# Kernel optimization log

Measured on AMD Instinct MI355X. Metric: run time of the kernel, lower is better.

## Reference

```python
import jax, jax.numpy as jnp
import numpy as np

NUM_HEADS = 16
HEAD_DIM = 64
LORA_SCALE = 1.0 / 8.0  # lora_alpha (1) / r (8), loralib defaults


def setup_inputs() -> dict:
    key = jax.random.key(0)
    ks = jax.random.split(key, 10)
    B, N, C = 4, 2048, 1024
    O = 3 * NUM_HEADS * HEAD_DIM  # 3072
    s = lambda fan: 1.0 / np.sqrt(fan)
    return {
        "x": jax.random.normal(ks[0], (B, N, C), jnp.float32),
        "W_qkv": jax.random.normal(ks[1], (O, C), jnp.float32) * s(C),
        "W_lora": jax.random.normal(ks[2], (O, C), jnp.float32) * s(C),
        "b_lora": jax.random.normal(ks[3], (O,), jnp.float32) * s(C),
        "A_q": jax.random.normal(ks[4], (8, C), jnp.float32) * s(C),
        "B_q": jnp.zeros((NUM_HEADS * HEAD_DIM, 8), jnp.float32) + jax.random.normal(ks[5], (NUM_HEADS * HEAD_DIM, 8), jnp.float32) * 0.02,
        "A_v": jax.random.normal(ks[6], (8, C), jnp.float32) * s(C),
        "B_v": jax.random.normal(ks[7], (NUM_HEADS * HEAD_DIM, 8), jnp.float32) * 0.02,
        "W_out": jax.random.normal(ks[8], (C, NUM_HEADS * HEAD_DIM), jnp.float32) * s(NUM_HEADS * HEAD_DIM),
        "b_out": jax.random.normal(ks[9], (C,), jnp.float32) * s(NUM_HEADS * HEAD_DIM),
    }


def reference(x, W_qkv, W_lora, b_lora, A_q, B_q, A_v, B_v, W_out, b_out):
    B, N, C = x.shape
    H, D = NUM_HEADS, HEAD_DIM
    scale = D ** (-0.5)

    def split_qkv(t):
        t = t.reshape(B, N, 3, H, D).transpose(2, 0, 3, 1, 4)
        return t[0], t[1], t[2]

    q, k, v = split_qkv(jnp.einsum('bnc,oc->bno', x, W_qkv))
    ql, _, vl = split_qkv(jnp.einsum('bnc,oc->bno', x, W_lora) + b_lora)

    # low-rank LoRA updates for Q and V slices only (K disabled)
    dq = (jnp.einsum('bnc,rc->bnr', x, A_q) @ B_q.T) * LORA_SCALE  # (B,N,HD)
    dv = (jnp.einsum('bnc,rc->bnr', x, A_v) @ B_v.T) * LORA_SCALE
    dq = dq.reshape(B, N, H, D).transpose(0, 2, 1, 3)
    dv = dv.reshape(B, N, H, D).transpose(0, 2, 1, 3)

    q = q + ql + dq
    v = v + vl + dv

    attn = jax.nn.softmax(jnp.einsum('bhnd,bhmd->bhnm', q, k) * scale, axis=-1)
    out = jnp.einsum('bhnm,bhmd->bhnd', attn, v)
    out = out.transpose(0, 2, 1, 3).reshape(B, N, H * D)  # b h n d -> b n (h d)
    return jnp.einsum('bnk,ck->bnc', out, W_out) + b_out
```

## Files before the change

kernel.cpp:

```cpp
#include <hip/hip_runtime.h>
#include <hip/hip_bf16.h>

typedef unsigned short u16;
typedef unsigned int u32;
typedef __attribute__((ext_vector_type(8))) short bf16x8;
typedef __attribute__((ext_vector_type(4))) float f32x4;

#define GLDS16(gptr, lptr)                                                        \
  __builtin_amdgcn_global_load_lds(                                               \
      (__attribute__((address_space(1))) const void*)(gptr),                      \
      (__attribute__((address_space(3))) void*)(lptr), 16, 0, 0)

__device__ __forceinline__ u16 f2bf(float f) {
  union { float f; unsigned u; } v; v.f = f;
  unsigned r = v.u + 0x7fffu + ((v.u >> 16) & 1u);
  return (u16)(r >> 16);
}

__device__ __forceinline__ u32 pack_bf2(float a, float b) {
  union { __hip_bfloat162 h2; u32 u; } v;
  v.h2 = __float22bfloat162_rn(make_float2(a, b));
  return v.u;
}

__global__ void k_f32_to_bf16(const float* __restrict__ in, u16* __restrict__ out, int n4) {
  int i = blockIdx.x * 256 + threadIdx.x;
  if (i < n4) {
    float4 f = reinterpret_cast<const float4*>(in)[i];
    ushort4 u;
    u.x = f2bf(f.x); u.y = f2bf(f.y); u.z = f2bf(f.z); u.w = f2bf(f.w);
    reinterpret_cast<ushort4*>(out)[i] = u;
  }
}

__global__ void k_prep_weff(const float* __restrict__ Wqkv, const float* __restrict__ Wlora,
                            const float* __restrict__ blora,
                            const float* __restrict__ Aq, const float* __restrict__ Bq,
                            const float* __restrict__ Av, const float* __restrict__ Bv,
                            u16* __restrict__ Weff, float* __restrict__ beff) {
  int idx = blockIdx.x * 256 + threadIdx.x;
  int o = idx >> 10, c = idx & 1023;
  float w = Wqkv[idx];
  if (o < 1024) {
    float lr = 0.f;
#pragma unroll
    for (int r = 0; r < 8; ++r) lr += Bq[o * 8 + r] * Aq[r * 1024 + c];
    w += Wlora[idx] + 0.125f * lr;
  } else if (o >= 2048) {
    int o2 = o - 2048;
    float lr = 0.f;
#pragma unroll
    for (int r = 0; r < 8; ++r) lr += Bv[o2 * 8 + r] * Av[r * 1024 + c];
    w += Wlora[idx] + 0.125f * lr;
  }
  Weff[idx] = f2bf(w);
  if (c == 0) beff[o] = (o < 1024 || o >= 2048) ? blora[o] : 0.f;
}

__global__ __launch_bounds__(256, 2)
void k_gemm_qkv(const u16* __restrict__ Xb, const u16* __restrict__ Weff,
                const float* __restrict__ beff, u16* __restrict__ Y) {
  __shared__ u16 As[128 * 32], Bs[128 * 32];
  const int tid = threadIdx.x, lane = tid & 63, wave = tid >> 6;
  const int lr = lane & 15, lg = lane >> 4;
  const int wr = wave >> 1, wc = wave & 1;
  const int m0 = blockIdx.y * 128, n0 = blockIdx.x * 128;
  f32x4 acc[4][4] = {};

  for (int k0 = 0; k0 < 1024; k0 += 32) {
#pragma unroll
    for (int i = 0; i < 2; ++i) {
      int gc = ((tid & 3) ^ ((tid >> 2) & 3)) << 3;
      GLDS16(Xb + (size_t)(m0 + i * 64 + (tid >> 2)) * 1024 + k0 + gc, As + i * 2048 + wave * 512);
      GLDS16(Weff + (size_t)(n0 + i * 64 + (tid >> 2)) * 1024 + k0 + gc, Bs + i * 2048 + wave * 512);
    }
    __syncthreads();
    bf16x8 af[4], bfr[4];
#pragma unroll
    for (int t = 0; t < 4; ++t) {
      int ch = ((lg ^ (lr & 3)) & 3) << 3;
      af[t]  = *reinterpret_cast<const bf16x8*>(As + (wr * 64 + t * 16 + lr) * 32 + ch);
      bfr[t] = *reinterpret_cast<const bf16x8*>(Bs + (wc * 64 + t * 16 + lr) * 32 + ch);
    }
#pragma unroll
    for (int mi = 0; mi < 4; ++mi)
#pragma unroll
      for (int ni = 0; ni < 4; ++ni)
        acc[mi][ni] = __builtin_amdgcn_mfma_f32_16x16x32_bf16(af[mi], bfr[ni], acc[mi][ni], 0, 0, 0);
    __syncthreads();
  }

#pragma unroll
  for (int mi = 0; mi < 4; ++mi) {
    int row = m0 + wr * 64 + mi * 16 + (lg << 2);
#pragma unroll
    for (int ni = 0; ni < 4; ++ni) {
      int col = n0 + wc * 64 + ni * 16 + lr;
      float bias = beff[col];
#pragma unroll
      for (int j = 0; j < 4; ++j) {
        float v = acc[mi][ni][j] + bias;
        if (col < 1024) v *= 0.18033688011112042f;
        Y[(size_t)(row + j) * 3072 + col] = f2bf(v);
      }
    }
  }
}

__global__ __launch_bounds__(256)
void k_vtrans(const u16* __restrict__ Y, u16* __restrict__ Vt) {
  __shared__ u16 Ls[64 * 65];
  const int t = threadIdx.x;
  const int bh = blockIdx.y, b = bh >> 4, h = bh & 15;
  const int n0 = blockIdx.x * 64;
#pragma unroll
  for (int c = 0; c < 2; ++c) {
    int idx = c * 256 + t;
    int nl = idx >> 3, d0 = (idx & 7) * 8;
    bf16x8 val = *reinterpret_cast<const bf16x8*>(
        Y + (size_t)(b * 2048 + n0 + nl) * 3072 + 2048 + h * 64 + d0);
#pragma unroll
    for (int j = 0; j < 8; ++j) Ls[(d0 + j) * 65 + nl] = (u16)val[j];
  }
  __syncthreads();
#pragma unroll
  for (int c = 0; c < 2; ++c) {
    int idx = c * 256 + t;
    int dl = idx >> 3, nn = (idx & 7) * 8;
    bf16x8 outv;
#pragma unroll
    for (int j = 0; j < 8; ++j) outv[j] = (short)Ls[dl * 65 + nn + j];
    *reinterpret_cast<bf16x8*>(Vt + (size_t)(bh * 64 + dl) * 2048 + n0 + nn) = outv;
  }
}

__global__ __launch_bounds__(256, 3)
void k_attn(const u16* __restrict__ Y, const u16* __restrict__ Vt, u16* __restrict__ Oa) {
  __shared__ u16 Ks[2][64 * 64], Vs[2][64 * 64];
  __shared__ u32 Pp[4 * 16 * 32];
  const int tid = threadIdx.x, lane = tid & 63, wave = tid >> 6;
  const int b = blockIdx.y >> 4, h = blockIdx.y & 15;
  const int q0 = blockIdx.x * 128;
  const int lr = lane & 15, lg = lane >> 4;
  const size_t bq = (size_t)b * 2048;
  const size_t bv = (size_t)b * 1024 + h * 64;
  const int hc = h * 64;

  bf16x8 qa[2][2];
#pragma unroll
  for (int g = 0; g < 2; ++g) {
    size_t row = bq + q0 + wave * 32 + g * 16 + lr;
#pragma unroll
    for (int hf = 0; hf < 2; ++hf)
      qa[g][hf] = *reinterpret_cast<const bf16x8*>(Y + row * 3072 + hc + hf * 32 + lg * 8);
  }

  float m_run[2] = {-1e30f, -1e30f}, l_run[2] = {0.f, 0.f};
  f32x4 oacc[2][4] = {};

  const int sr = tid >> 3, sc = tid & 7;
  const u32 pbase = wave * 512 + lr * 32;
  const u32 pswz  = (lr & 7) << 4;

  auto stage = [&](int key0, int bb) {
#pragma unroll
    for (int i = 0; i < 2; ++i) {
      int r = i * 32 + sr;
      int gc = (sc ^ (r & 7)) << 3;
      GLDS16(Y + (bq + key0 + r) * 3072 + 1024 + hc + gc, &Ks[bb][i * 2048 + wave * 512]);
      GLDS16(Vt + (bv + r) * 2048 + key0 + gc,            &Vs[bb][i * 2048 + wave * 512]);
    }
  };

  stage(0, 0);
  for (int kt = 0; kt < 32; ++kt) {
    const int cur = kt & 1;
    if (kt < 31) {
      stage((kt + 1) * 64, cur ^ 1);
      asm volatile("s_waitcnt vmcnt(4)" ::: "memory");
    } else {
      asm volatile("s_waitcnt vmcnt(0)" ::: "memory");
    }
    __builtin_amdgcn_s_barrier();
    asm volatile("" ::: "memory");

    bf16x8 kb[4][2], vb[4][2];
#pragma unroll
    for (int s = 0; s < 4; ++s) {
      int row = s * 16 + lr;
#pragma unroll
      for (int hf = 0; hf < 2; ++hf) {
        int ch = ((hf * 4 + lg) ^ (row & 7)) << 3;
        kb[s][hf] = *reinterpret_cast<const bf16x8*>(&Ks[cur][row * 64 + ch]);
        vb[s][hf] = *reinterpret_cast<const bf16x8*>(&Vs[cur][row * 64 + ch]);
      }
    }

#pragma unroll
    for (int g = 0; g < 2; ++g) {
      f32x4 p4[4] = {};
      __builtin_amdgcn_s_setprio(1);
#pragma unroll
      for (int s = 0; s < 4; ++s)
#pragma unroll
        for (int hf = 0; hf < 2; ++hf)
          p4[s] = __builtin_amdgcn_mfma_f32_16x16x32_bf16(kb[s][hf], qa[g][hf], p4[s], 0, 0, 0);
      __builtin_amdgcn_s_setprio(0);

      float ma = fmaxf(fmaxf(p4[0][0], p4[0][1]), fmaxf(p4[0][2], p4[0][3]));
      float mb = fmaxf(fmaxf(p4[1][0], p4[1][1]), fmaxf(p4[1][2], p4[1][3]));
      float mc = fmaxf(fmaxf(p4[2][0], p4[2][1]), fmaxf(p4[2][2], p4[2][3]));
      float md = fmaxf(fmaxf(p4[3][0], p4[3][1]), fmaxf(p4[3][2], p4[3][3]));
      float tmax = fmaxf(fmaxf(ma, mb), fmaxf(mc, md));
      tmax = fmaxf(tmax, __shfl_xor(tmax, 16));
      tmax = fmaxf(tmax, __shfl_xor(tmax, 32));

      if (__any(tmax > m_run[g] + 11.0f)) {
        float mnew = fmaxf(m_run[g], tmax);
        float alpha = __builtin_amdgcn_exp2f(m_run[g] - mnew);
        m_run[g] = mnew;
        l_run[g] *= alpha;
        float abc[4];
#pragma unroll
        for (int j = 0; j < 4; ++j) abc[j] = __shfl(alpha, (lg << 2) + j);
#pragma unroll
        for (int dt = 0; dt < 4; ++dt)
#pragma unroll
          for (int j = 0; j < 4; ++j) oacc[g][dt][j] *= abc[j];
      }

      float rs = 0.f;
      u32 w[4][2];
#pragma unroll
      for (int s = 0; s < 4; ++s) {
        float e0 = __builtin_amdgcn_exp2f(p4[s][0] - m_run[g]);
        float e1 = __builtin_amdgcn_exp2f(p4[s][1] - m_run[g]);
        float e2 = __builtin_amdgcn_exp2f(p4[s][2] - m_run[g]);
        float e3 = __builtin_amdgcn_exp2f(p4[s][3] - m_run[g]);
        rs += (e0 + e1) + (e2 + e3);
        w[s][0] = pack_bf2(e0, e1);
        w[s][1] = pack_bf2(e2, e3);
      }
      rs += __shfl_xor(rs, 16);
      rs += __shfl_xor(rs, 32);
      l_run[g] += rs;

#pragma unroll
      for (int s = 0; s < 4; ++s) {
        u32 ui = pbase + ((((u32)(s * 32 + lg * 8)) ^ pswz) >> 2);
        *reinterpret_cast<uint2*>(&Pp[ui]) = make_uint2(w[s][0], w[s][1]);
      }
      asm volatile("s_waitcnt lgkmcnt(0)" ::: "memory");
      __builtin_amdgcn_sched_barrier(0);

      __builtin_amdgcn_s_setprio(1);
#pragma unroll
      for (int kk = 0; kk < 2; ++kk) {
        u32 ur = pbase + ((((u32)(kk * 64 + lg * 16)) ^ pswz) >> 2);
        bf16x8 pa = *reinterpret_cast<const bf16x8*>(&Pp[ur]);
#pragma unroll
        for (int dt = 0; dt < 4; ++dt)
          oacc[g][dt] = __builtin_amdgcn_mfma_f32_16x16x32_bf16(pa, vb[dt][kk], oacc[g][dt], 0, 0, 0);
      }
      __builtin_amdgcn_s_setprio(0);
    }
    asm volatile("" ::: "memory");
    __builtin_amdgcn_s_barrier();
  }

#pragma unroll
  for (int g = 0; g < 2; ++g) {
    float lbc[4];
#pragma unroll
    for (int j = 0; j < 4; ++j)
      lbc[j] = __builtin_amdgcn_rcpf(__shfl(l_run[g], (lg << 2) + j));
    int rowb = (int)bq + q0 + wave * 32 + g * 16 + (lg << 2);
#pragma unroll
    for (int dt = 0; dt < 4; ++dt) {
      int col = hc + dt * 16 + lr;
#pragma unroll
      for (int j = 0; j < 4; ++j) {
        float v = oacc[g][dt][j] * lbc[j];
        Oa[(size_t)(rowb + j) * 1024 + col] = f2bf(v);
      }
    }
  }
}

__global__ __launch_bounds__(256, 2)
void k_gemm_out(const u16* __restrict__ Ob, const u16* __restrict__ Wb,
                const float* __restrict__ bout, float* __restrict__ out) {
  __shared__ u16 As[128 * 32], Bs[128 * 32];
  const int tid = threadIdx.x, lane = tid & 63, wave = tid >> 6;
  const int lr = lane & 15, lg = lane >> 4;
  const int wr = wave >> 1, wc = wave & 1;
  const int m0 = blockIdx.y * 128, n0 = blockIdx.x * 128;
  f32x4 acc[4][4] = {};

  for (int k0 = 0; k0 < 1024; k0 += 32) {
#pragma unroll
    for (int i = 0; i < 2; ++i) {
      int gc = ((tid & 3) ^ ((tid >> 2) & 3)) << 3;
      GLDS16(Ob + (size_t)(m0 + i * 64 + (tid >> 2)) * 1024 + k0 + gc, As + i * 2048 + wave * 512);
      GLDS16(Wb + (size_t)(n0 + i * 64 + (tid >> 2)) * 1024 + k0 + gc, Bs + i * 2048 + wave * 512);
    }
    __syncthreads();
    bf16x8 af[4], bfr[4];
#pragma unroll
    for (int t = 0; t < 4; ++t) {
      int ch = ((lg ^ (lr & 3)) & 3) << 3;
      af[t]  = *reinterpret_cast<const bf16x8*>(As + (wr * 64 + t * 16 + lr) * 32 + ch);
      bfr[t] = *reinterpret_cast<const bf16x8*>(Bs + (wc * 64 + t * 16 + lr) * 32 + ch);
    }
#pragma unroll
    for (int mi = 0; mi < 4; ++mi)
#pragma unroll
      for (int ni = 0; ni < 4; ++ni)
        acc[mi][ni] = __builtin_amdgcn_mfma_f32_16x16x32_bf16(af[mi], bfr[ni], acc[mi][ni], 0, 0, 0);
    __syncthreads();
  }

#pragma unroll
  for (int mi = 0; mi < 4; ++mi) {
    int row = m0 + wr * 64 + mi * 16 + (lg << 2);
#pragma unroll
    for (int ni = 0; ni < 4; ++ni) {
      int col = n0 + wc * 64 + ni * 16 + lr;
      float bias = bout[col];
#pragma unroll
      for (int j = 0; j < 4; ++j)
        out[(size_t)(row + j) * 1024 + col] = acc[mi][ni][j] + bias;
    }
  }
}

extern "C" void kernel_launch(void* const* d_in, const int* in_sizes, int n_in,
                              void* d_out, int out_size, void* d_ws, size_t ws_size,
                              hipStream_t stream) {
  const float* x     = (const float*)d_in[0];
  const float* Wqkv  = (const float*)d_in[1];
  const float* Wlora = (const float*)d_in[2];
  const float* blora = (const float*)d_in[3];
  const float* Aq    = (const float*)d_in[4];
  const float* Bq    = (const float*)d_in[5];
  const float* Av    = (const float*)d_in[6];
  const float* Bv    = (const float*)d_in[7];
  const float* Wout  = (const float*)d_in[8];
  const float* bout  = (const float*)d_in[9];
  float* out = (float*)d_out;

  char* w = (char*)d_ws;
  auto alloc = [&](size_t bytes) { char* p = w; w += (bytes + 255) & ~(size_t)255; return p; };
  u16*   Xb    = (u16*)alloc((size_t)8192 * 1024 * 2);
  u16*   Weff  = (u16*)alloc((size_t)3072 * 1024 * 2);
  float* beff  = (float*)alloc((size_t)3072 * 4);
  u16*   Woutb = (u16*)alloc((size_t)1024 * 1024 * 2);
  u16*   Y     = (u16*)alloc((size_t)8192 * 3072 * 2);
  u16*   Vt    = (u16*)alloc((size_t)4096 * 1024 * 2 * 2);
  u16*   Oa    = Xb;

  k_f32_to_bf16<<<dim3(8192), dim3(256), 0, stream>>>(x, Xb, 8192 * 1024 / 4);
  k_f32_to_bf16<<<dim3(1024), dim3(256), 0, stream>>>(Wout, Woutb, 1024 * 1024 / 4);
  k_prep_weff<<<dim3(12288), dim3(256), 0, stream>>>(Wqkv, Wlora, blora, Aq, Bq, Av, Bv, Weff, beff);
  k_gemm_qkv<<<dim3(24, 64), dim3(256), 0, stream>>>(Xb, Weff, beff, Y);
  k_vtrans<<<dim3(32, 64), dim3(256), 0, stream>>>(Y, Vt);
  k_attn<<<dim3(16, 64), dim3(256), 0, stream>>>(Y, Vt, Oa);
  k_gemm_out<<<dim3(8, 64), dim3(256), 0, stream>>>(Oa, Woutb, bout, out);
}
```

Before: 347.4 us.

## Switch attention to 32x32x16 MFMA and pass P via permlane32_swap instead of LDS

The attention kernel now uses 32x32x16 bf16 MFMAs in place of 16x16x32, so each wave covers its 32 query rows with one tile instead of two 16-row groups. This changes the register layout of Q, K and V fragments and of the output accumulator, and needs only one running max and sum per lane. The softmax probabilities are rearranged into the A-operand layout with permlane32_swap, which removes the LDS scratch buffer, its stores, the lgkmcnt wait and the reload. The aim is fewer MFMA issues, less LDS traffic and lower sync overhead in the inner loop. The new layout has to be exactly right for correctness, and register pressure may change.

Measured after the change: 335.5 us. -3.4%, faster.

```diff
diff --git a/kernel.cpp b/kernel.cpp
--- a/kernel.cpp
+++ b/kernel.cpp
@@ -5,6 +5,7 @@
 typedef unsigned int u32;
 typedef __attribute__((ext_vector_type(8))) short bf16x8;
 typedef __attribute__((ext_vector_type(4))) float f32x4;
+typedef __attribute__((ext_vector_type(16))) float f32x16;
 
 #define GLDS16(gptr, lptr)                                                        \
   __builtin_amdgcn_global_load_lds(                                               \
@@ -137,31 +138,26 @@
 __global__ __launch_bounds__(256, 3)
 void k_attn(const u16* __restrict__ Y, const u16* __restrict__ Vt, u16* __restrict__ Oa) {
   __shared__ u16 Ks[2][64 * 64], Vs[2][64 * 64];
-  __shared__ u32 Pp[4 * 16 * 32];
   const int tid = threadIdx.x, lane = tid & 63, wave = tid >> 6;
   const int b = blockIdx.y >> 4, h = blockIdx.y & 15;
   const int q0 = blockIdx.x * 128;
-  const int lr = lane & 15, lg = lane >> 4;
+  const int l31 = lane & 31, hi = lane >> 5;
   const size_t bq = (size_t)b * 2048;
   const size_t bv = (size_t)b * 1024 + h * 64;
   const int hc = h * 64;
 
-  bf16x8 qa[2][2];
-#pragma unroll
-  for (int g = 0; g < 2; ++g) {
-    size_t row = bq + q0 + wave * 32 + g * 16 + lr;
-#pragma unroll
-    for (int hf = 0; hf < 2; ++hf)
-      qa[g][hf] = *reinterpret_cast<const bf16x8*>(Y + row * 3072 + hc + hf * 32 + lg * 8);
-  }
-
-  float m_run[2] = {-1e30f, -1e30f}, l_run[2] = {0.f, 0.f};
-  f32x4 oacc[2][4] = {};
+  bf16x8 qb[4];
+  {
+    const u16* yr = Y + (bq + q0 + wave * 32 + l31) * 3072 + hc + hi * 8;
+#pragma unroll
+    for (int ks = 0; ks < 4; ++ks)
+      qb[ks] = *reinterpret_cast<const bf16x8*>(yr + ks * 16);
+  }
+
+  float m_run = -1e30f, l_run = 0.f;
+  f32x16 oacc[2] = {};
 
   const int sr = tid >> 3, sc = tid & 7;
-  const u32 pbase = wave * 512 + lr * 32;
-  const u32 pswz  = (lr & 7) << 4;
-
   auto stage = [&](int key0, int bb) {
 #pragma unroll
     for (int i = 0; i < 2; ++i) {
@@ -184,106 +180,105 @@
     __builtin_amdgcn_s_barrier();
     asm volatile("" ::: "memory");
 
-    bf16x8 kb[4][2], vb[4][2];
-#pragma unroll
-    for (int s = 0; s < 4; ++s) {
-      int row = s * 16 + lr;
-#pragma unroll
-      for (int hf = 0; hf < 2; ++hf) {
-        int ch = ((hf * 4 + lg) ^ (row & 7)) << 3;
-        kb[s][hf] = *reinterpret_cast<const bf16x8*>(&Ks[cur][row * 64 + ch]);
-        vb[s][hf] = *reinterpret_cast<const bf16x8*>(&Vs[cur][row * 64 + ch]);
+    bf16x8 kb[2][4], vb[2][4];
+#pragma unroll
+    for (int t = 0; t < 2; ++t) {
+      const u16* kbase = &Ks[cur][(t * 32 + l31) * 64];
+      int rx = (t * 32 + l31) & 7;
+#pragma unroll
+      for (int ks = 0; ks < 4; ++ks)
+        kb[t][ks] = *reinterpret_cast<const bf16x8*>(kbase + (((ks * 2 + hi) ^ rx) << 3));
+    }
+#pragma unroll
+    for (int dt = 0; dt < 2; ++dt) {
+      const u16* vbase = &Vs[cur][(dt * 32 + l31) * 64];
+      int rx = (dt * 32 + l31) & 7;
+#pragma unroll
+      for (int ks = 0; ks < 4; ++ks)
+        vb[dt][ks] = *reinterpret_cast<const bf16x8*>(vbase + (((ks * 2 + hi) ^ rx) << 3));
+    }
+
+    f32x16 p4[2] = {};
+    __builtin_amdgcn_s_setprio(1);
+#pragma unroll
+    for (int t = 0; t < 2; ++t)
+#pragma unroll
+      for (int ks = 0; ks < 4; ++ks)
+        p4[t] = __builtin_amdgcn_mfma_f32_32x32x16_bf16(kb[t][ks], qb[ks], p4[t], 0, 0, 0);
+    __builtin_amdgcn_s_setprio(0);
+
+    float mx[8];
+#pragma unroll
+    for (int r = 0; r < 8; ++r)
+      mx[r] = fmaxf(fmaxf(p4[0][r], p4[0][r + 8]), fmaxf(p4[1][r], p4[1][r + 8]));
+#pragma unroll
+    for (int s = 4; s > 0; s >>= 1)
+#pragma unroll
+      for (int r = 0; r < s; ++r) mx[r] = fmaxf(mx[r], mx[r + s]);
+    float tmax = fmaxf(mx[0], __shfl_xor(mx[0], 32));
+
+    if (__any(tmax > m_run + 11.0f)) {
+      float mnew = fmaxf(m_run, tmax);
+      float alpha = __builtin_amdgcn_exp2f(m_run - mnew);
+      m_run = mnew;
+      l_run *= alpha;
+#pragma unroll
+      for (int r = 0; r < 16; ++r) {
+        float ab = __shfl(alpha, (r & 3) + 8 * (r >> 2) + 4 * hi);
+        oacc[0][r] *= ab;
+        oacc[1][r] *= ab;
       }
     }
 
-#pragma unroll
-    for (int g = 0; g < 2; ++g) {
-      f32x4 p4[4] = {};
-      __builtin_amdgcn_s_setprio(1);
-#pragma unroll
-      for (int s = 0; s < 4; ++s)
-#pragma unroll
-        for (int hf = 0; hf < 2; ++hf)
-          p4[s] = __builtin_amdgcn_mfma_f32_16x16x32_bf16(kb[s][hf], qa[g][hf], p4[s], 0, 0, 0);
-      __builtin_amdgcn_s_setprio(0);
-
-      float ma = fmaxf(fmaxf(p4[0][0], p4[0][1]), fmaxf(p4[0][2], p4[0][3]));
-      float mb = fmaxf(fmaxf(p4[1][0], p4[1][1]), fmaxf(p4[1][2], p4[1][3]));
-      float mc = fmaxf(fmaxf(p4[2][0], p4[2][1]), fmaxf(p4[2][2], p4[2][3]));
-      float md = fmaxf(fmaxf(p4[3][0], p4[3][1]), fmaxf(p4[3][2], p4[3][3]));
-      float tmax = fmaxf(fmaxf(ma, mb), fmaxf(mc, md));
-      tmax = fmaxf(tmax, __shfl_xor(tmax, 16));
-      tmax = fmaxf(tmax, __shfl_xor(tmax, 32));
-
-      if (__any(tmax > m_run[g] + 11.0f)) {
-        float mnew = fmaxf(m_run[g], tmax);
-        float alpha = __builtin_amdgcn_exp2f(m_run[g] - mnew);
-        m_run[g] = mnew;
-        l_run[g] *= alpha;
-        float abc[4];
-#pragma unroll
-        for (int j = 0; j < 4; ++j) abc[j] = __shfl(alpha, (lg << 2) + j);
-#pragma unroll
-        for (int dt = 0; dt < 4; ++dt)
-#pragma unroll
-          for (int j = 0; j < 4; ++j) oacc[g][dt][j] *= abc[j];
+    float rs = 0.f;
+    u32 w[2][4][2];
+#pragma unroll
+    for (int t = 0; t < 2; ++t)
+#pragma unroll
+      for (int g = 0; g < 4; ++g) {
+        float e0 = __builtin_amdgcn_exp2f(p4[t][4 * g + 0] - m_run);
+        float e1 = __builtin_amdgcn_exp2f(p4[t][4 * g + 1] - m_run);
+        float e2 = __builtin_amdgcn_exp2f(p4[t][4 * g + 2] - m_run);
+        float e3 = __builtin_amdgcn_exp2f(p4[t][4 * g + 3] - m_run);
+        rs += (e0 + e1) + (e2 + e3);
+        w[t][g][0] = pack_bf2(e0, e1);
+        w[t][g][1] = pack_bf2(e2, e3);
       }
-
-      float rs = 0.f;
-      u32 w[4][2];
-#pragma unroll
-      for (int s = 0; s < 4; ++s) {
-        float e0 = __builtin_amdgcn_exp2f(p4[s][0] - m_run[g]);
-        float e1 = __builtin_amdgcn_exp2f(p4[s][1] - m_run[g]);
-        float e2 = __builtin_amdgcn_exp2f(p4[s][2] - m_run[g]);
-        float e3 = __builtin_amdgcn_exp2f(p4[s][3] - m_run[g]);
-        rs += (e0 + e1) + (e2 + e3);
-        w[s][0] = pack_bf2(e0, e1);
-        w[s][1] = pack_bf2(e2, e3);
-      }
-      rs += __shfl_xor(rs, 16);
-      rs += __shfl_xor(rs, 32);
-      l_run[g] += rs;
-
-#pragma unroll
-      for (int s = 0; s < 4; ++s) {
-        u32 ui = pbase + ((((u32)(s * 32 + lg * 8)) ^ pswz) >> 2);
-        *reinterpret_cast<uint2*>(&Pp[ui]) = make_uint2(w[s][0], w[s][1]);
-      }
-      asm volatile("s_waitcnt lgkmcnt(0)" ::: "memory");
-      __builtin_amdgcn_sched_barrier(0);
-
-      __builtin_amdgcn_s_setprio(1);
-#pragma unroll
-      for (int kk = 0; kk < 2; ++kk) {
-        u32 ur = pbase + ((((u32)(kk * 64 + lg * 16)) ^ pswz) >> 2);
-        bf16x8 pa = *reinterpret_cast<const bf16x8*>(&Pp[ur]);
-#pragma unroll
-        for (int dt = 0; dt < 4; ++dt)
-          oacc[g][dt] = __builtin_amdgcn_mfma_f32_16x16x32_bf16(pa, vb[dt][kk], oacc[g][dt], 0, 0, 0);
-      }
-      __builtin_amdgcn_s_setprio(0);
-    }
+    rs += __shfl_xor(rs, 32);
+    l_run += rs;
+
+    bf16x8 pa[4];
+#pragma unroll
+    for (int ks = 0; ks < 4; ++ks) {
+      const int t = ks >> 1, q2 = (ks & 1) * 2;
+      auto s0 = __builtin_amdgcn_permlane32_swap(w[t][q2][0], w[t][q2 + 1][0], false, false);
+      auto s1 = __builtin_amdgcn_permlane32_swap(w[t][q2][1], w[t][q2 + 1][1], false, false);
+      union { u32 u[4]; bf16x8 v; } cv;
+      cv.u[0] = s0[0]; cv.u[1] = s1[0]; cv.u[2] = s0[1]; cv.u[3] = s1[1];
+      pa[ks] = cv.v;
+    }
+
+    __builtin_amdgcn_s_setprio(1);
+#pragma unroll
+    for (int ks = 0; ks < 4; ++ks) {
+      oacc[0] = __builtin_amdgcn_mfma_f32_32x32x16_bf16(pa[ks], vb[0][ks], oacc[0], 0, 0, 0);
+      oacc[1] = __builtin_amdgcn_mfma_f32_32x32x16_bf16(pa[ks], vb[1][ks], oacc[1], 0, 0, 0);
+    }
+    __builtin_amdgcn_s_setprio(0);
+
     asm volatile("" ::: "memory");
     __builtin_amdgcn_s_barrier();
   }
 
-#pragma unroll
-  for (int g = 0; g < 2; ++g) {
-    float lbc[4];
-#pragma unroll
-    for (int j = 0; j < 4; ++j)
-      lbc[j] = __builtin_amdgcn_rcpf(__shfl(l_run[g], (lg << 2) + j));
-    int rowb = (int)bq + q0 + wave * 32 + g * 16 + (lg << 2);
-#pragma unroll
-    for (int dt = 0; dt < 4; ++dt) {
-      int col = hc + dt * 16 + lr;
-#pragma unroll
-      for (int j = 0; j < 4; ++j) {
-        float v = oacc[g][dt][j] * lbc[j];
-        Oa[(size_t)(rowb + j) * 1024 + col] = f2bf(v);
-      }
-    }
+  float linv = __builtin_amdgcn_rcpf(l_run);
+  const size_t orow0 = bq + q0 + wave * 32;
+#pragma unroll
+  for (int r = 0; r < 16; ++r) {
+    int qr = (r & 3) + 8 * (r >> 2) + 4 * hi;
+    float li = __shfl(linv, qr);
+    size_t rb = (orow0 + qr) * 1024 + hc + l31;
+    Oa[rb]      = f2bf(oacc[0][r] * li);
+    Oa[rb + 32] = f2bf(oacc[1][r] * li);
   }
 }
 
```
